# Performance work log

Hardware: AMD Instinct MI355X
Metric: run time of the kernel (lower is better)

## Reference

```python
import jax, jax.numpy as jnp
import numpy as np

T, B, C, H, W = 9, 8, 256, 56, 56


def setup_inputs() -> dict:
    key = jax.random.key(0)
    k1, k2, k3, k4 = jax.random.split(key, 4)
    feature_maps_sequence = jax.random.normal(k1, (T, B, C, H, W), dtype=jnp.float32)
    # Conv2d(2C, 1, kernel_size=1): weight [1, 2C, 1, 1], bias [1]
    w = jax.random.normal(k2, (1, 2 * C, 1, 1), dtype=jnp.float32) * 0.02
    b = jax.random.normal(k3, (1,), dtype=jnp.float32) * 0.02
    gamma = jax.random.normal(k4, (1,), dtype=jnp.float32)
    return {"feature_maps_sequence": feature_maps_sequence, "w": w, "b": b, "gamma": gamma}


def reference(feature_maps_sequence, w, b, gamma):
    seq = feature_maps_sequence  # [T, B, C, H, W]
    t = seq.shape[0]
    center = seq[t // 2]  # [B, C, H, W]
    c = seq.shape[2]
    # 1x1 conv over concat([center, frame]) == dot with split weight halves + bias
    w_center = w[0, :c, 0, 0]  # [C]
    w_other = w[0, c:, 0, 0]   # [C]
    score_center = jnp.einsum('bchw,c->bhw', center, w_center)          # [B, H, W]
    score_other = jnp.einsum('tbchw,c->tbhw', seq, w_other)             # [T, B, H, W]
    scores = score_center[None] + score_other + b[0]                    # [T, B, H, W]
    attn = jax.nn.softmax(scores, axis=0)                               # softmax over T
    attended = jnp.einsum('tbhw,tbchw->bchw', attn, seq)                # [B, C, H, W]
    return center + gamma * attended
```

## Files before the change

kernel.cpp:

```cpp
#include <hip/hip_runtime.h>
#include <math.h>

#define TT 9
#define BN 8
#define CC 256
#define HW 3136
#define PX 32
#define NW (HW / PX)
#define CI 32
#define CJ (CC / CI)
#define CENTER_T 4
#define PSTR (TT * PX + 4)

__global__ __launch_bounds__(256, 4) void fused_stream_kernel(
    const float* __restrict__ seq, const float* __restrict__ w,
    const float* __restrict__ gamma, float* __restrict__ out) {
  const int blk = blockIdx.x;
  const int b = blk & 7;
  const int wdw = blk >> 3;
  const int px0 = wdw * PX;
  const int tid = threadIdx.x;
  const int ci = tid >> 3;
  const int ui = tid & 7;

  __shared__ __align__(16) float part[CI * PSTR];
  __shared__ float scr[TT * PX];
  __shared__ __align__(16) float attn[TT * PX];

  float wreg[CJ];
#pragma unroll
  for (int j = 0; j < CJ; ++j) wreg[j] = w[CC + ci + CI * j];

  const float* base0 = seq + ((size_t)b * CC + ci) * HW + px0 + 4 * ui;

  float4 acc[TT];
#pragma unroll
  for (int t = 0; t < TT; ++t) acc[t] = make_float4(0.f, 0.f, 0.f, 0.f);

#pragma unroll
  for (int j = 0; j < CJ; ++j) {
    const float wj = wreg[j];
#pragma unroll
    for (int t = 0; t < TT; ++t) {
      const float4 v =
          *(const float4*)(base0 + (size_t)t * (BN * CC * HW) + (size_t)j * (CI * HW));
      acc[t].x = fmaf(wj, v.x, acc[t].x);
      acc[t].y = fmaf(wj, v.y, acc[t].y);
      acc[t].z = fmaf(wj, v.z, acc[t].z);
      acc[t].w = fmaf(wj, v.w, acc[t].w);
    }
  }
#pragma unroll
  for (int t = 0; t < TT; ++t)
    *(float4*)(&part[ci * PSTR + t * PX + ui * 4]) = acc[t];
  __syncthreads();

  for (int v = tid; v < TT * PX; v += 256) {
    float s = 0.f;
#pragma unroll
    for (int c2 = 0; c2 < CI; ++c2) s += part[c2 * PSTR + v];
    scr[v] = s;
  }
  __syncthreads();

  if (tid < PX) {
    float vv[TT];
    float m = -1e30f;
#pragma unroll
    for (int t = 0; t < TT; ++t) {
      const float s = scr[t * PX + tid];
      vv[t] = s;
      m = fmaxf(m, s);
    }
    float s = 0.f;
#pragma unroll
    for (int t = 0; t < TT; ++t) { vv[t] = __expf(vv[t] - m); s += vv[t]; }
    const float inv = 1.f / s;
#pragma unroll
    for (int t = 0; t < TT; ++t) attn[t * PX + tid] = vv[t] * inv;
  }
  __syncthreads();

  float4 at[TT];
#pragma unroll
  for (int t = 0; t < TT; ++t)
    at[t] = *(const float4*)(&attn[t * PX + ui * 4]);

  const float gm = gamma[0];
#pragma unroll
  for (int j = 0; j < CJ; ++j) {
    float4 o = make_float4(0.f, 0.f, 0.f, 0.f);
    float4 cv = make_float4(0.f, 0.f, 0.f, 0.f);
#pragma unroll
    for (int t = 0; t < TT; ++t) {
      const float4 v =
          *(const float4*)(base0 + (size_t)t * (BN * CC * HW) + (size_t)j * (CI * HW));
      o.x = fmaf(at[t].x, v.x, o.x);
      o.y = fmaf(at[t].y, v.y, o.y);
      o.z = fmaf(at[t].z, v.z, o.z);
      o.w = fmaf(at[t].w, v.w, o.w);
      if (t == CENTER_T) cv = v;
    }
    float4 r;
    r.x = fmaf(gm, o.x, cv.x);
    r.y = fmaf(gm, o.y, cv.y);
    r.z = fmaf(gm, o.z, cv.z);
    r.w = fmaf(gm, o.w, cv.w);
    float* ob = out + ((size_t)b * CC + ci + CI * j) * HW + px0 + 4 * ui;
    *(float4*)(ob) = r;
  }
}

extern "C" void kernel_launch(void* const* d_in, const int* in_sizes, int n_in,
                              void* d_out, int out_size, void* d_ws, size_t ws_size,
                              hipStream_t stream) {
  const float* seq = (const float*)d_in[0];
  const float* w = (const float*)d_in[1];
  const float* gamma = (const float*)d_in[3];
  float* out = (float*)d_out;

  fused_stream_kernel<<<BN * NW, 256, 0, stream>>>(seq, w, gamma, out);
}
```

Measured before the change: 371.4 us.

## Stage sequence tile once in LDS as bf16 to avoid second global read

The kernel now loads each block's 9x256x32 slice of the sequence from global memory once, converts it to bf16 and keeps it in shared memory. Both the score reduction and the attention-weighted sum then read from LDS, instead of streaming the input from global memory twice. To fit the tile, blocks grow to 1024 threads with about 150KB of LDS, so only one block fits per CU and there is no overlap between the load and compute phases. The bf16 rounding also reaches the output through the center term and the weighted sum, which risks accuracy-tolerance failures.

Result: faster. 341.9 us (-8.0%).

```diff
diff --git a/kernel.cpp b/kernel.cpp
--- a/kernel.cpp
+++ b/kernel.cpp
@@ -7,12 +7,17 @@
 #define HW 3136
 #define PX 32
 #define NW (HW / PX)
-#define CI 32
-#define CJ (CC / CI)
 #define CENTER_T 4
-#define PSTR (TT * PX + 4)
 
-__global__ __launch_bounds__(256, 4) void fused_stream_kernel(
+__device__ __forceinline__ unsigned int bfr(float x) {
+  unsigned int u = __float_as_uint(x);
+  return (u + 0x7fffu + ((u >> 16) & 1u)) >> 16;
+}
+__device__ __forceinline__ unsigned int pkbf(float lo, float hi) {
+  return bfr(lo) | (bfr(hi) << 16);
+}
+
+__global__ __launch_bounds__(1024) void fused_bf16_kernel(
     const float* __restrict__ seq, const float* __restrict__ w,
     const float* __restrict__ gamma, float* __restrict__ out) {
   const int blk = blockIdx.x;
@@ -20,46 +25,64 @@
   const int wdw = blk >> 3;
   const int px0 = wdw * PX;
   const int tid = threadIdx.x;
-  const int ci = tid >> 3;
-  const int ui = tid & 7;
 
-  __shared__ __align__(16) float part[CI * PSTR];
+  __shared__ unsigned short tile16[TT * CC * PX];
+  __shared__ float wsh[CC];
+  __shared__ float red[TT * 16 * 4 * 2];
   __shared__ float scr[TT * PX];
-  __shared__ __align__(16) float attn[TT * PX];
+  __shared__ __align__(16) float attnF[TT * PX];
 
-  float wreg[CJ];
+  if (tid < CC) wsh[tid] = w[CC + tid];
+
+  {
+    const int ui = tid & 7;
+    const int cq = tid >> 3;
 #pragma unroll
-  for (int j = 0; j < CJ; ++j) wreg[j] = w[CC + ci + CI * j];
-
-  const float* base0 = seq + ((size_t)b * CC + ci) * HW + px0 + 4 * ui;
-
-  float4 acc[TT];
+    for (int h = 0; h < 2; ++h) {
+      const int c = cq + h * 128;
+      const float* gp = seq + ((size_t)b * CC + c) * HW + px0 + 4 * ui;
+      float4 v[TT];
 #pragma unroll
-  for (int t = 0; t < TT; ++t) acc[t] = make_float4(0.f, 0.f, 0.f, 0.f);
-
+      for (int t = 0; t < TT; ++t)
+        v[t] = *(const float4*)(gp + (size_t)t * (BN * CC * HW));
 #pragma unroll
-  for (int j = 0; j < CJ; ++j) {
-    const float wj = wreg[j];
-#pragma unroll
-    for (int t = 0; t < TT; ++t) {
-      const float4 v =
-          *(const float4*)(base0 + (size_t)t * (BN * CC * HW) + (size_t)j * (CI * HW));
-      acc[t].x = fmaf(wj, v.x, acc[t].x);
-      acc[t].y = fmaf(wj, v.y, acc[t].y);
-      acc[t].z = fmaf(wj, v.z, acc[t].z);
-      acc[t].w = fmaf(wj, v.w, acc[t].w);
+      for (int t = 0; t < TT; ++t) {
+        uint2 pk;
+        pk.x = pkbf(v[t].x, v[t].y);
+        pk.y = pkbf(v[t].z, v[t].w);
+        *(uint2*)(&tile16[(t * CC + c) * PX + 4 * ui]) = pk;
+      }
     }
   }
-#pragma unroll
-  for (int t = 0; t < TT; ++t)
-    *(float4*)(&part[ci * PSTR + t * PX + ui * 4]) = acc[t];
   __syncthreads();
 
-  for (int v = tid; v < TT * PX; v += 256) {
-    float s = 0.f;
+  if (tid < 576) {
+    const int cp = tid & 3;
+    const int item = tid >> 2;
+    const int t = item >> 4;
+    const int p = item & 15;
+    const unsigned int* tp = (const unsigned int*)tile16;
+    float sA = 0.f, sB = 0.f;
 #pragma unroll
-    for (int c2 = 0; c2 < CI; ++c2) s += part[c2 * PSTR + v];
-    scr[v] = s;
+    for (int i = 0; i < 64; ++i) {
+      const int c = cp + 4 * i;
+      const unsigned int u = tp[(t * CC + c) * (PX / 2) + p];
+      const float fe = __uint_as_float(u << 16);
+      const float fo = __uint_as_float(u & 0xffff0000u);
+      const float wv = wsh[c];
+      sA = fmaf(wv, fe, sA);
+      sB = fmaf(wv, fo, sB);
+    }
+    red[(item * 4 + cp) * 2 + 0] = sA;
+    red[(item * 4 + cp) * 2 + 1] = sB;
+  }
+  __syncthreads();
+
+  if (tid < TT * PX) {
+    const int t = tid >> 5;
+    const int px = tid & 31;
+    const int base = (t * 16 + (px >> 1)) * 8 + (px & 1);
+    scr[tid] = red[base] + red[base + 2] + red[base + 4] + red[base + 6];
   }
   __syncthreads();
 
@@ -68,46 +91,62 @@
     float m = -1e30f;
 #pragma unroll
     for (int t = 0; t < TT; ++t) {
-      const float s = scr[t * PX + tid];
-      vv[t] = s;
-      m = fmaxf(m, s);
+      vv[t] = scr[t * PX + tid];
+      m = fmaxf(m, vv[t]);
     }
     float s = 0.f;
 #pragma unroll
     for (int t = 0; t < TT; ++t) { vv[t] = __expf(vv[t] - m); s += vv[t]; }
     const float inv = 1.f / s;
 #pragma unroll
-    for (int t = 0; t < TT; ++t) attn[t * PX + tid] = vv[t] * inv;
+    for (int t = 0; t < TT; ++t) attnF[t * PX + tid] = vv[t] * inv;
   }
   __syncthreads();
 
-  float4 at[TT];
-#pragma unroll
-  for (int t = 0; t < TT; ++t)
-    at[t] = *(const float4*)(&attn[t * PX + ui * 4]);
-
-  const float gm = gamma[0];
-#pragma unroll
-  for (int j = 0; j < CJ; ++j) {
-    float4 o = make_float4(0.f, 0.f, 0.f, 0.f);
-    float4 cv = make_float4(0.f, 0.f, 0.f, 0.f);
+  {
+    const int ui = tid & 3;
+    const int c = tid >> 2;
+    float4 oA = {0.f, 0.f, 0.f, 0.f}, oB = {0.f, 0.f, 0.f, 0.f};
+    float4 cA = {0.f, 0.f, 0.f, 0.f}, cB = {0.f, 0.f, 0.f, 0.f};
 #pragma unroll
     for (int t = 0; t < TT; ++t) {
-      const float4 v =
-          *(const float4*)(base0 + (size_t)t * (BN * CC * HW) + (size_t)j * (CI * HW));
-      o.x = fmaf(at[t].x, v.x, o.x);
-      o.y = fmaf(at[t].y, v.y, o.y);
-      o.z = fmaf(at[t].z, v.z, o.z);
-      o.w = fmaf(at[t].w, v.w, o.w);
-      if (t == CENTER_T) cv = v;
+      const int base = (t * CC + c) * PX + 4 * ui;
+      const uint2 ua = *(const uint2*)(&tile16[base]);
+      const uint2 ub = *(const uint2*)(&tile16[base + 16]);
+      const float4 sA = *(const float4*)(&attnF[t * PX + 4 * ui]);
+      const float4 sB = *(const float4*)(&attnF[t * PX + 16 + 4 * ui]);
+      float4 va, vb;
+      va.x = __uint_as_float(ua.x << 16);
+      va.y = __uint_as_float(ua.x & 0xffff0000u);
+      va.z = __uint_as_float(ua.y << 16);
+      va.w = __uint_as_float(ua.y & 0xffff0000u);
+      vb.x = __uint_as_float(ub.x << 16);
+      vb.y = __uint_as_float(ub.x & 0xffff0000u);
+      vb.z = __uint_as_float(ub.y << 16);
+      vb.w = __uint_as_float(ub.y & 0xffff0000u);
+      oA.x = fmaf(sA.x, va.x, oA.x);
+      oA.y = fmaf(sA.y, va.y, oA.y);
+      oA.z = fmaf(sA.z, va.z, oA.z);
+      oA.w = fmaf(sA.w, va.w, oA.w);
+      oB.x = fmaf(sB.x, vb.x, oB.x);
+      oB.y = fmaf(sB.y, vb.y, oB.y);
+      oB.z = fmaf(sB.z, vb.z, oB.z);
+      oB.w = fmaf(sB.w, vb.w, oB.w);
+      if (t == CENTER_T) { cA = va; cB = vb; }
     }
-    float4 r;
-    r.x = fmaf(gm, o.x, cv.x);
-    r.y = fmaf(gm, o.y, cv.y);
-    r.z = fmaf(gm, o.z, cv.z);
-    r.w = fmaf(gm, o.w, cv.w);
-    float* ob = out + ((size_t)b * CC + ci + CI * j) * HW + px0 + 4 * ui;
-    *(float4*)(ob) = r;
+    const float gm = gamma[0];
+    float4 rA, rB;
+    rA.x = fmaf(gm, oA.x, cA.x);
+    rA.y = fmaf(gm, oA.y, cA.y);
+    rA.z = fmaf(gm, oA.z, cA.z);
+    rA.w = fmaf(gm, oA.w, cA.w);
+    rB.x = fmaf(gm, oB.x, cB.x);
+    rB.y = fmaf(gm, oB.y, cB.y);
+    rB.z = fmaf(gm, oB.z, cB.z);
+    rB.w = fmaf(gm, oB.w, cB.w);
+    float* ob = out + ((size_t)b * CC + c) * HW + px0 + 4 * ui;
+    *(float4*)(ob) = rA;
+    *(float4*)(ob + 16) = rB;
   }
 }
 
@@ -119,5 +158,5 @@
   const float* gamma = (const float*)d_in[3];
   float* out = (float*)d_out;
 
-  fused_stream_kernel<<<BN * NW, 256, 0, stream>>>(seq, w, gamma, out);
+  fused_bf16_kernel<<<BN * NW, 1024, 0, stream>>>(seq, w, gamma, out);
 }
```
